# Performance work log

Hardware: AMD Instinct MI355X
Metric: run time of the kernel (lower is better)

The kernel has to match this reference:

```python
import jax, jax.numpy as jnp
import numpy as np

B, L, D, H, NL = 16, 256, 768, 12, 4
HD = D // H          # head size = 64; also edge-feature embedding dim
V, E, C, F = 30000, 50, 2, 3072
CLS_ID = 1


def _pos_emb(length, dim):
    # standard sinusoidal positional embedding [L, D]
    pos = jnp.arange(length, dtype=jnp.float32)[:, None]
    div = jnp.exp(-np.log(10000.0) * jnp.arange(0, dim, 2, dtype=jnp.float32) / dim)
    ang = pos * div[None, :]
    pe = jnp.zeros((length, dim), jnp.float32)
    return pe.at[:, 0::2].set(jnp.sin(ang)).at[:, 1::2].set(jnp.cos(ang))


def _ln(x, g, b, eps=1e-5):
    m = x.mean(-1, keepdims=True)
    v = x.var(-1, keepdims=True)
    return (x - m) * jax.lax.rsqrt(v + eps) * g + b


def setup_inputs() -> dict:
    key = jax.random.key(0)
    ks = jax.random.split(key, 16)
    s = 0.02
    word_ids = jax.random.randint(ks[0], (B, L), 0, V).at[:, 0].set(CLS_ID)
    batched_adj = jax.random.bernoulli(ks[1], 0.3, (B, L, L)) | jnp.eye(L, dtype=bool)[None]
    edge_types = jax.random.randint(ks[2], (B, L, L), 0, E)
    word_emb = (jax.random.normal(ks[3], (V, D)) * s).at[0].set(0.0)   # padding_idx=0
    edge_emb = (jax.random.normal(ks[4], (E, HD)) * s).at[0].set(0.0)  # padding_idx=0
    pw = lambda k, shp: jax.random.normal(k, shp) * s
    return {
        "word_ids": word_ids, "batched_adj": batched_adj, "edge_types": edge_types,
        "word_emb": word_emb, "edge_emb": edge_emb,
        "Wq": pw(ks[5], (NL, D, D)), "bq": jnp.zeros((NL, D)),
        "Wk": pw(ks[6], (NL, D, D)), "bk": jnp.zeros((NL, D)),
        "Wv": pw(ks[7], (NL, D, D)), "bv": jnp.zeros((NL, D)),
        "Wo": pw(ks[8], (NL, D, D)), "bo": jnp.zeros((NL, D)),
        "ln1_g": jnp.ones((NL, D)), "ln1_b": jnp.zeros((NL, D)),
        "W1": pw(ks[9], (NL, D, F)), "b1": jnp.zeros((NL, F)),
        "W2": pw(ks[10], (NL, F, D)), "b2": jnp.zeros((NL, D)),
        "ln2_g": jnp.ones((NL, D)), "ln2_b": jnp.zeros((NL, D)),
        "cls_W": pw(ks[11], (D, C)), "cls_b": jnp.zeros((C,)),
    }


def reference(word_ids, batched_adj, edge_types, word_emb, edge_emb,
              Wq, bq, Wk, bk, Wv, bv, Wo, bo, ln1_g, ln1_b,
              W1, b1, W2, b2, ln2_g, ln2_b, cls_W, cls_b):
    # node features: word embedding + positional embedding
    h = word_emb[word_ids] + _pos_emb(L, D)[None]          # [B,L,D]
    scale = 1.0 / np.sqrt(HD)
    eemb = edge_emb[edge_types]                             # [B,L,L,HD] edge key features
    neg = jnp.asarray(-1e9, h.dtype)
    mask = batched_adj[:, None]                             # [B,1,L,L]
    for l in range(NL):
        q = (h @ Wq[l] + bq[l]).reshape(B, L, H, HD)
        k = (h @ Wk[l] + bk[l]).reshape(B, L, H, HD)
        v = (h @ Wv[l] + bv[l]).reshape(B, L, H, HD)
        # scores: node-node + query . edge-key-feature, adjacency-masked
        scores = jnp.einsum('bihd,bjhd->bhij', q, k)
        scores = scores + jnp.einsum('bihd,bijd->bhij', q, eemb)
        scores = jnp.where(mask, scores * scale, neg)
        att = jax.nn.softmax(scores, axis=-1)               # [B,H,L,L]
        out = jnp.einsum('bhij,bjhd->bihd', att, v).reshape(B, L, D)
        h = _ln(h + (out @ Wo[l] + bo[l]), ln1_g[l], ln1_b[l])
        ff = jax.nn.relu(h @ W1[l] + b1[l]) @ W2[l] + b2[l]
        h = _ln(h + ff, ln2_g[l], ln2_b[l])
    cls_h = h[:, 0]                                         # CLS pooling
    logits = cls_h @ cls_W + cls_b                          # [B,C]
    return logits
```

## Files before the change

### kernel.cpp

```cpp
#include <hip/hip_runtime.h>
#include <hip/hip_bf16.h>

#define BB 16
#define LL 256
#define DD 768
#define HH 12
#define HDD 64
#define NLL 4
#define FF 3072
#define EE 50
#define QKVS 2304
#define TOKD ((size_t)BB * LL * DD)

typedef unsigned short ushort_t;
typedef __bf16 bf16x8 __attribute__((ext_vector_type(8)));
typedef float f32x4 __attribute__((ext_vector_type(4)));

__device__ __forceinline__ float b2f(ushort_t u) {
    union { unsigned int i; float f; } x; x.i = ((unsigned int)u) << 16; return x.f;
}
__device__ __forceinline__ ushort_t f2b(float f) {
    unsigned int u = __builtin_bit_cast(unsigned int, f);
    unsigned int r = u + 0x7fffu + ((u >> 16) & 1u);
    return (ushort_t)(r >> 16);
}

__device__ __forceinline__ void gl2lds16(const void* g, void* l) {
    __builtin_amdgcn_global_load_lds(
        (const __attribute__((address_space(1))) unsigned int*)g,
        (__attribute__((address_space(3))) unsigned int*)l,
        16, 0, 0);
}

__global__ __launch_bounds__(256) void transpose_f2b(
    const float* __restrict__ in, ushort_t* __restrict__ out, int R, int C,
    long inZ, long outZ)
{
    __shared__ ushort_t tile[32][33];
    in  += (long)blockIdx.z * inZ;
    out += (long)blockIdx.z * outZ;
    int c0 = blockIdx.x * 32, r0 = blockIdx.y * 32;
    int tx = threadIdx.x, ty = threadIdx.y;
#pragma unroll
    for (int i = 0; i < 32; i += 8)
        tile[ty + i][tx] = f2b(in[(long)(r0 + ty + i) * C + c0 + tx]);
    __syncthreads();
#pragma unroll
    for (int i = 0; i < 32; i += 8)
        out[(long)(c0 + ty + i) * R + r0 + tx] = tile[tx][ty + i];
}

__global__ __launch_bounds__(256) void fuse_bias_kernel(
    const float* __restrict__ bq, const float* __restrict__ bk,
    const float* __restrict__ bv, int l, float* __restrict__ out)
{
    int n = blockIdx.x * 256 + threadIdx.x;
    if (n >= QKVS) return;
    float v = (n < DD) ? bq[l * DD + n]
            : (n < 2 * DD) ? bk[l * DD + n - DD]
            : bv[l * DD + n - 2 * DD];
    out[n] = v;
}

__global__ __launch_bounds__(256) void embed_kernel(
    const int* __restrict__ wids, const float* __restrict__ wemb,
    float* __restrict__ hf, ushort_t* __restrict__ hb)
{
    long idx = (long)blockIdx.x * 256 + threadIdx.x;
    int d = (int)(idx % DD);
    int t = (int)(idx / DD);
    int lpos = t & (LL - 1);
    int wid = wids[t];
    float freq = expf(-9.210340371976184f * (float)(d & ~1) * (1.f / (float)DD));
    float ang = (float)lpos * freq;
    float pe = (d & 1) ? cosf(ang) : sinf(ang);
    float hv = wemb[(long)wid * DD + d] + pe;
    hf[idx] = hv;
    hb[idx] = f2b(hv);
}

__global__ __launch_bounds__(256) void gemm_bf16(
    const ushort_t* __restrict__ A, const ushort_t* __restrict__ Bt,
    const float* __restrict__ bias,
    ushort_t* __restrict__ outb, float* __restrict__ outf,
    int M, int N, int K, int Ksl, int relu)
{
    __shared__ __align__(16) ushort_t As[3][128 * 32];
    __shared__ __align__(16) ushort_t Bs[3][128 * 32];
    const int tid = threadIdx.x;
    const int wave = tid >> 6, lane = tid & 63;
    const int quad = lane >> 4, l16 = lane & 15;
    const int m0 = blockIdx.y * 128, n0 = blockIdx.x * 128;
    const int z = blockIdx.z;
    const int kbase = z * Ksl;
    const int wm = (wave >> 1) * 64, wn = (wave & 1) * 64;
    const ushort_t* Ab = A + (long)m0 * K;
    const ushort_t* Bb = Bt + (long)n0 * K;

    const int srow = tid >> 2, skc = (tid & 3) * 8;

    f32x4 acc[4][4];
#pragma unroll
    for (int mi = 0; mi < 4; ++mi)
#pragma unroll
        for (int ni = 0; ni < 4; ++ni) acc[mi][ni] = (f32x4){0.f, 0.f, 0.f, 0.f};

    const int nk = Ksl >> 5;

    auto stage = [&](int kt, ushort_t* Ad, ushort_t* Bd) {
        const int k0 = kbase + (kt << 5);
        const ushort_t* ga = &Ab[(long)srow * K + k0 + skc];
        const ushort_t* gb = &Bb[(long)srow * K + k0 + skc];
        char* la = (char*)Ad + wave * 1024;
        char* lb = (char*)Bd + wave * 1024;
        gl2lds16(ga, la);
        gl2lds16(gb, lb);
        gl2lds16(ga + (long)64 * K, la + 4096);
        gl2lds16(gb + (long)64 * K, lb + 4096);
    };

    ushort_t *A0 = As[0], *A1 = As[1], *A2 = As[2];
    ushort_t *B0 = Bs[0], *B1 = Bs[1], *B2 = Bs[2];

    stage(0, A0, B0);
    stage(1, A1, B1);

    for (int kt = 0; kt < nk; ++kt) {
        if (kt + 1 < nk) {
            asm volatile("s_waitcnt vmcnt(4)" ::: "memory");
        } else {
            asm volatile("s_waitcnt vmcnt(0)" ::: "memory");
        }
        __builtin_amdgcn_s_barrier();
        __builtin_amdgcn_sched_barrier(0);
        if (kt + 2 < nk) stage(kt + 2, A2, B2);
        bf16x8 af[4], bfr[4];
#pragma unroll
        for (int t = 0; t < 4; ++t)
            af[t] = *(const bf16x8*)&A0[(wm + t * 16 + l16) * 32 + quad * 8];
#pragma unroll
        for (int t = 0; t < 4; ++t)
            bfr[t] = *(const bf16x8*)&B0[(wn + t * 16 + l16) * 32 + quad * 8];
#pragma unroll
        for (int mi = 0; mi < 4; ++mi)
#pragma unroll
            for (int ni = 0; ni < 4; ++ni)
                acc[mi][ni] = __builtin_amdgcn_mfma_f32_16x16x32_bf16(
                    af[mi], bfr[ni], acc[mi][ni], 0, 0, 0);
        ushort_t* ta = A0; A0 = A1; A1 = A2; A2 = ta;
        ushort_t* tb = B0; B0 = B1; B1 = B2; B2 = tb;
    }

    float* outfz = outf ? outf + (size_t)z * M * N : nullptr;
#pragma unroll
    for (int ni = 0; ni < 4; ++ni) {
        int col = n0 + wn + ni * 16 + l16;
        float bv = (bias && z == 0) ? bias[col] : 0.f;
#pragma unroll
        for (int mi = 0; mi < 4; ++mi) {
#pragma unroll
            for (int r = 0; r < 4; ++r) {
                int row = m0 + wm + mi * 16 + quad * 4 + r;
                float vv = acc[mi][ni][r] + bv;
                if (relu) vv = fmaxf(vv, 0.f);
                if (outb) outb[(long)row * N + col] = f2b(vv);
                if (outfz) outfz[(long)row * N + col] = vv;
            }
        }
    }
}

#define QS_STR 72
#define VT_STR 264
#define P_STR  264
#define S_STR  257
#define PE_STR 53

__global__ __launch_bounds__(256) void attn_kernel(
    const ushort_t* __restrict__ qkv,
    const int* __restrict__ adjm, const int* __restrict__ etyp,
    const float* __restrict__ eemb, ushort_t* __restrict__ out)
{
    __shared__ __align__(16) char smem[64448];
    ushort_t* VT = (ushort_t*)smem;
    float*    S  = (float*)(smem + 33792);
    ushort_t* P  = (ushort_t*)(smem + 50240);
    float*    Pe = (float*)(smem + 58688);
    char*     U  = smem + 62080;
    float* invrow = (float*)(smem + 64384);
    ushort_t* Qs = (ushort_t*)U;
    float*    red = (float*)U;

    const int blk = blockIdx.x;
    const int qt = blk & 15;
    const int h  = (blk >> 4) % HH;
    const int b  = blk / (16 * HH);
    const int i0 = qt * 16;
    const int tid = threadIdx.x;
    const int wave = tid >> 6, lane = tid & 63;
    const int quad = lane >> 4, l16 = lane & 15;

    if (tid < 128) {
        int row = tid >> 3, d0 = (tid & 7) * 8;
        *(int4*)&Qs[row * QS_STR + d0] =
            *(const int4*)&qkv[((long)(b * LL + i0 + row)) * QKVS + h * HDD + d0];
    }
#pragma unroll
    for (int i = 0; i < 8; ++i) {
        int c = tid + i * 256;
        int j = c >> 3, d0 = (c & 7) * 8;
        int4 raw = *(const int4*)&qkv[((long)(b * LL + j)) * QKVS + 2 * DD + h * HDD + d0];
        const ushort_t* vals = (const ushort_t*)&raw;
#pragma unroll
        for (int u = 0; u < 8; ++u) VT[(d0 + u) * VT_STR + j] = vals[u];
    }
    __syncthreads();

    {
        int e = wave * 16 + l16;
        f32x4 acc = (f32x4){0.f, 0.f, 0.f, 0.f};
#pragma unroll
        for (int kk = 0; kk < 2; ++kk) {
            bf16x8 af = *(const bf16x8*)&Qs[l16 * QS_STR + kk * 32 + quad * 8];
            bf16x8 bf = (bf16x8){0, 0, 0, 0, 0, 0, 0, 0};
            if (e < EE) {
                const float* ep = &eemb[(long)e * HDD + kk * 32 + quad * 8];
#pragma unroll
                for (int u = 0; u < 8; ++u) bf[u] = (__bf16)ep[u];
            }
            acc = __builtin_amdgcn_mfma_f32_16x16x32_bf16(af, bf, acc, 0, 0, 0);
        }
        if (e < EE) {
#pragma unroll
            for (int r = 0; r < 4; ++r) Pe[(quad * 4 + r) * PE_STR + e] = acc[r];
        }
    }

#pragma unroll
    for (int jt = 0; jt < 4; ++jt) {
        int jtile = wave * 4 + jt;
        int j = jtile * 16 + l16;
        f32x4 acc = (f32x4){0.f, 0.f, 0.f, 0.f};
#pragma unroll
        for (int kk = 0; kk < 2; ++kk) {
            bf16x8 af = *(const bf16x8*)&Qs[l16 * QS_STR + kk * 32 + quad * 8];
            bf16x8 bf = *(const bf16x8*)&qkv[((long)(b * LL + j)) * QKVS + DD + h * HDD + kk * 32 + quad * 8];
            acc = __builtin_amdgcn_mfma_f32_16x16x32_bf16(af, bf, acc, 0, 0, 0);
        }
#pragma unroll
        for (int r = 0; r < 4; ++r)
            S[(quad * 4 + r) * S_STR + jtile * 16 + l16] = acc[r];
    }
    __syncthreads();

    {
        const int row = tid & 15, seg = tid >> 4;
        const int i = i0 + row;
        const int* etp = etyp + ((long)(b * LL + i)) * LL + seg * 16;
        const int* adp = adjm + ((long)(b * LL + i)) * LL + seg * 16;
        int etv[16], adv[16];
#pragma unroll
        for (int t = 0; t < 4; ++t) {
            *(int4*)&etv[t * 4] = *(const int4*)&etp[t * 4];
            *(int4*)&adv[t * 4] = *(const int4*)&adp[t * 4];
        }
        float vals[16];
        float pmax = -1e30f;
#pragma unroll
        for (int c = 0; c < 16; ++c) {
            float s = S[row * S_STR + seg * 16 + c];
            float pe = Pe[row * PE_STR + etv[c]];
            float vv = adv[c] ? (s + pe) * 0.125f : -1e30f;
            vals[c] = vv;
            pmax = fmaxf(pmax, vv);
        }
        red[row * 17 + seg] = pmax;
        __syncthreads();
        float m = -1e30f;
#pragma unroll
        for (int g = 0; g < 16; ++g) m = fmaxf(m, red[row * 17 + g]);
        float sum = 0.f;
#pragma unroll
        for (int c = 0; c < 16; ++c) {
            float p = __expf(vals[c] - m);
            ushort_t pb = f2b(p);
            sum += b2f(pb);
            P[row * P_STR + seg * 16 + c] = pb;
        }
        red[272 + row * 17 + seg] = sum;
        __syncthreads();
        if (tid < 16) {
            float tot = 0.f;
#pragma unroll
            for (int g = 0; g < 16; ++g) tot += red[272 + tid * 17 + g];
            invrow[tid] = 1.f / tot;
        }
        __syncthreads();
    }

    {
        f32x4 acc = (f32x4){0.f, 0.f, 0.f, 0.f};
#pragma unroll
        for (int kt = 0; kt < 8; ++kt) {
            bf16x8 af = *(const bf16x8*)&P[l16 * P_STR + kt * 32 + quad * 8];
            bf16x8 bf = *(const bf16x8*)&VT[(wave * 16 + l16) * VT_STR + kt * 32 + quad * 8];
            acc = __builtin_amdgcn_mfma_f32_16x16x32_bf16(af, bf, acc, 0, 0, 0);
        }
#pragma unroll
        for (int r = 0; r < 4; ++r) {
            int row = quad * 4 + r;
            float ov = acc[r] * invrow[row];
            out[((long)(b * LL + i0 + row)) * DD + h * HDD + wave * 16 + l16] = f2b(ov);
        }
    }
}

__global__ __launch_bounds__(256) void ln_kernel(
    float* __restrict__ hf, ushort_t* __restrict__ hb,
    const float* __restrict__ proj, int nparts,
    const float* __restrict__ g, const float* __restrict__ be)
{
    const int r = blockIdx.x, tid = threadIdx.x;
    const long rb = (long)r * DD;
    float x[3];
#pragma unroll
    for (int i = 0; i < 3; ++i) {
        int d = tid + i * 256;
        float t = hf[rb + d];
        for (int p = 0; p < nparts; ++p) t += proj[(size_t)p * TOKD + rb + d];
        x[i] = t;
    }
    float s = x[0] + x[1] + x[2];
    float s2 = x[0] * x[0] + x[1] * x[1] + x[2] * x[2];
#pragma unroll
    for (int o = 1; o < 64; o <<= 1) { s += __shfl_xor(s, o); s2 += __shfl_xor(s2, o); }
    __shared__ float rs[4], rq[4];
    int wave = tid >> 6;
    if ((tid & 63) == 0) { rs[wave] = s; rq[wave] = s2; }
    __syncthreads();
    float S  = rs[0] + rs[1] + rs[2] + rs[3];
    float S2 = rq[0] + rq[1] + rq[2] + rq[3];
    float mean = S * (1.f / (float)DD);
    float var  = S2 * (1.f / (float)DD) - mean * mean;
    float rstd = rsqrtf(var + 1e-5f);
#pragma unroll
    for (int i = 0; i < 3; ++i) {
        int d = tid + i * 256;
        float y = (x[i] - mean) * rstd * g[d] + be[d];
        hf[rb + d] = y;
        hb[rb + d] = f2b(y);
    }
}

__global__ __launch_bounds__(256) void cls_kernel(
    const float* __restrict__ hf, const float* __restrict__ W,
    const float* __restrict__ bias, float* __restrict__ out)
{
    int b = blockIdx.x, tid = threadIdx.x;
    const float* hr = hf + (long)b * LL * DD;
    float p0 = 0.f, p1 = 0.f;
    for (int d = tid; d < DD; d += 256) {
        float hv = hr[d];
        p0 = fmaf(hv, W[d * 2 + 0], p0);
        p1 = fmaf(hv, W[d * 2 + 1], p1);
    }
#pragma unroll
    for (int o = 1; o < 64; o <<= 1) { p0 += __shfl_xor(p0, o); p1 += __shfl_xor(p1, o); }
    __shared__ float r0[4], r1[4];
    int wave = tid >> 6;
    if ((tid & 63) == 0) { r0[wave] = p0; r1[wave] = p1; }
    __syncthreads();
    if (tid == 0) {
        out[b * 2 + 0] = r0[0] + r0[1] + r0[2] + r0[3] + bias[0];
        out[b * 2 + 1] = r1[0] + r1[1] + r1[2] + r1[3] + bias[1];
    }
}

extern "C" void kernel_launch(void* const* d_in, const int* in_sizes, int n_in,
                              void* d_out, int out_size, void* d_ws, size_t ws_size,
                              hipStream_t stream)
{
    const int* word_ids = (const int*)d_in[0];
    const int* adjm     = (const int*)d_in[1];
    const int* etyp     = (const int*)d_in[2];
    const float* wemb   = (const float*)d_in[3];
    const float* eemb   = (const float*)d_in[4];
    const float* Wq     = (const float*)d_in[5];
    const float* bq     = (const float*)d_in[6];
    const float* Wk     = (const float*)d_in[7];
    const float* bk     = (const float*)d_in[8];
    const float* Wv     = (const float*)d_in[9];
    const float* bv     = (const float*)d_in[10];
    const float* Wo     = (const float*)d_in[11];
    const float* bo     = (const float*)d_in[12];
    const float* ln1g   = (const float*)d_in[13];
    const float* ln1b   = (const float*)d_in[14];
    const float* W1     = (const float*)d_in[15];
    const float* b1     = (const float*)d_in[16];
    const float* W2     = (const float*)d_in[17];
    const float* b2     = (const float*)d_in[18];
    const float* ln2g   = (const float*)d_in[19];
    const float* ln2b   = (const float*)d_in[20];
    const float* clsW   = (const float*)d_in[21];
    const float* clsb   = (const float*)d_in[22];
    float* outp = (float*)d_out;

    char* ws = (char*)d_ws;
    size_t off = 0;
    auto alloc = [&](size_t bytes) -> char* {
        char* p = ws + off;
        off += (bytes + 255) & ~(size_t)255;
        return p;
    };
    const size_t DxD = (size_t)DD * DD;
    const size_t DxF = (size_t)DD * FF;
    const size_t TOK = (size_t)BB * LL;
    const size_t LSTR = (size_t)QKVS * DD + DxD + 2 * DxF;

    float*    hf  = (float*)alloc(TOK * DD * 4);
    ushort_t* hb  = (ushort_t*)alloc(TOK * DD * 2);
    ushort_t* qkv = (ushort_t*)alloc(TOK * QKVS * 2);
    ushort_t* ao  = (ushort_t*)alloc(TOK * DD * 2);
    float*    pjf = (float*)alloc(TOK * DD * 4);
    ushort_t* tw  = (ushort_t*)alloc(DxF * 2);
    ushort_t* ff1 = qkv;
    size_t tier1 = off + TOK * DD * 4;
    size_t tier2 = tier1 + 2 * TOK * DD * 4;
    size_t tier3 = tier2 + NLL * LSTR * 2;
    int S_o = 1, S_f = 1;
    ushort_t* cache = nullptr;
    if (ws_size >= tier1) { (void)alloc(TOK * DD * 4); S_o = 2; S_f = 2; }
    if (ws_size >= tier2) { (void)alloc(2 * TOK * DD * 4); S_f = 4; }
    if (ws_size >= tier3) { cache = (ushort_t*)alloc(NLL * LSTR * 2); }
    (void)in_sizes; (void)n_in; (void)out_size;

    dim3 tb(32, 8, 1);
    if (cache) {
        transpose_f2b<<<dim3(24, 24, NLL), tb, 0, stream>>>(Wq, cache,                 DD, DD, DxD, LSTR);
        transpose_f2b<<<dim3(24, 24, NLL), tb, 0, stream>>>(Wk, cache + DD * DD,       DD, DD, DxD, LSTR);
        transpose_f2b<<<dim3(24, 24, NLL), tb, 0, stream>>>(Wv, cache + 2 * DD * DD,   DD, DD, DxD, LSTR);
        transpose_f2b<<<dim3(24, 24, NLL), tb, 0, stream>>>(Wo, cache + 3 * DD * DD,   DD, DD, DxD, LSTR);
        transpose_f2b<<<dim3(96, 24, NLL), tb, 0, stream>>>(W1, cache + 4 * DD * DD,   DD, FF, DxF, LSTR);
        transpose_f2b<<<dim3(24, 96, NLL), tb, 0, stream>>>(W2, cache + 4 * DD * DD + DxF, FF, DD, DxF, LSTR);
    }

    embed_kernel<<<(int)(TOK * DD / 256), 256, 0, stream>>>(word_ids, wemb, hf, hb);

    const int M = (int)TOK;
    for (int l = 0; l < NLL; ++l) {
        const ushort_t *BtQKV, *BtO, *BtW1, *BtW2;
        if (cache) {
            const ushort_t* base = cache + (size_t)l * LSTR;
            BtQKV = base; BtO = base + 3 * DD * DD;
            BtW1 = base + 4 * DD * DD; BtW2 = base + 4 * DD * DD + DxF;
        } else {
            BtQKV = tw; BtO = tw; BtW1 = tw; BtW2 = tw;
        }
        fuse_bias_kernel<<<9, 256, 0, stream>>>(bq, bk, bv, l, pjf);
        if (!cache) {
            transpose_f2b<<<dim3(24, 24), tb, 0, stream>>>(Wq + (size_t)l * DxD, tw,               DD, DD, 0, 0);
            transpose_f2b<<<dim3(24, 24), tb, 0, stream>>>(Wk + (size_t)l * DxD, tw + DD * DD,     DD, DD, 0, 0);
            transpose_f2b<<<dim3(24, 24), tb, 0, stream>>>(Wv + (size_t)l * DxD, tw + 2 * DD * DD, DD, DD, 0, 0);
        }
        gemm_bf16<<<dim3(QKVS / 128, M / 128, 1), 256, 0, stream>>>(
            hb, BtQKV, pjf, qkv, nullptr, M, QKVS, DD, DD, 0);
        attn_kernel<<<BB * HH * 16, 256, 0, stream>>>(qkv, adjm, etyp, eemb, ao);
        if (!cache)
            transpose_f2b<<<dim3(24, 24), tb, 0, stream>>>(Wo + (size_t)l * DxD, tw, DD, DD, 0, 0);
        gemm_bf16<<<dim3(DD / 128, M / 128, S_o), 256, 0, stream>>>(
            ao, BtO, bo + l * DD, nullptr, pjf, M, DD, DD, DD / S_o, 0);
        ln_kernel<<<M, 256, 0, stream>>>(hf, hb, pjf, S_o, ln1g + l * DD, ln1b + l * DD);
        if (!cache)
            transpose_f2b<<<dim3(96, 24), tb, 0, stream>>>(W1 + (size_t)l * DxF, tw, DD, FF, 0, 0);
        gemm_bf16<<<dim3(FF / 128, M / 128, 1), 256, 0, stream>>>(
            hb, BtW1, b1 + l * FF, ff1, nullptr, M, FF, DD, DD, 1);
        if (!cache)
            transpose_f2b<<<dim3(24, 96), tb, 0, stream>>>(W2 + (size_t)l * DxF, tw, FF, DD, 0, 0);
        gemm_bf16<<<dim3(DD / 128, M / 128, S_f), 256, 0, stream>>>(
            ff1, BtW2, b2 + l * DD, nullptr, pjf, M, DD, FF, FF / S_f, 0);
        ln_kernel<<<M, 256, 0, stream>>>(hf, hb, pjf, S_f, ln2g + l * DD, ln2b + l * DD);
    }
    cls_kernel<<<BB, 256, 0, stream>>>(hf, clsW, clsb, outp);
}
```

Measured before the change: 1.213 ms.

## Prefetch V and mask loads into registers, alias LDS, swizzle V transpose, remap blocks

The attention kernel now issues its global loads for V, edge types and adjacency at kernel start, holding them in registers so their latency overlaps the score computation. The V transpose into shared memory is deferred until after the softmax, which lets VT alias the S/Pe region and shrinks LDS from about 64KB to about 44KB, allowing more resident workgroups. VT writes and reads use an XOR swizzle to reduce bank conflicts. Block IDs are remapped so neighbouring workgroups spread across batch/head, which may change cache locality. The cost is much higher register pressure from the 8 int4 V values plus 32 ints held across phases.

```diff
diff --git a/kernel.cpp b/kernel.cpp
--- a/kernel.cpp
+++ b/kernel.cpp
@@ -176,22 +176,31 @@
 #define S_STR  257
 #define PE_STR 53
 
+#define SM_S    0
+#define SM_PE   16448
+#define SM_VT   0
+#define SM_P    33792
+#define SM_U    42240
+#define SM_INV  44544
+#define SM_SZ   44608
+
 __global__ __launch_bounds__(256) void attn_kernel(
     const ushort_t* __restrict__ qkv,
     const int* __restrict__ adjm, const int* __restrict__ etyp,
     const float* __restrict__ eemb, ushort_t* __restrict__ out)
 {
-    __shared__ __align__(16) char smem[64448];
-    ushort_t* VT = (ushort_t*)smem;
-    float*    S  = (float*)(smem + 33792);
-    ushort_t* P  = (ushort_t*)(smem + 50240);
-    float*    Pe = (float*)(smem + 58688);
-    char*     U  = smem + 62080;
-    float* invrow = (float*)(smem + 64384);
+    __shared__ __align__(16) char smem[SM_SZ];
+    float*    S  = (float*)(smem + SM_S);
+    float*    Pe = (float*)(smem + SM_PE);
+    ushort_t* VT = (ushort_t*)(smem + SM_VT);
+    ushort_t* P  = (ushort_t*)(smem + SM_P);
+    char*     U  = smem + SM_U;
+    float* invrow = (float*)(smem + SM_INV);
     ushort_t* Qs = (ushort_t*)U;
     float*    red = (float*)U;
 
-    const int blk = blockIdx.x;
+    const int wgid = blockIdx.x;
+    const int blk = (wgid & 7) * ((BB * HH * 16) / 8) + (wgid >> 3);
     const int qt = blk & 15;
     const int h  = (blk >> 4) % HH;
     const int b  = blk / (16 * HH);
@@ -200,19 +209,29 @@
     const int wave = tid >> 6, lane = tid & 63;
     const int quad = lane >> 4, l16 = lane & 15;
 
+    const int vd0 = (tid & 7) * 8;
+    const int vj0 = tid >> 3;
+    int4 vreg[8];
+#pragma unroll
+    for (int i = 0; i < 8; ++i)
+        vreg[i] = *(const int4*)&qkv[((long)(b * LL + vj0 + 32 * i)) * QKVS + 2 * DD + h * HDD + vd0];
+
+    const int arow = tid & 15, aseg = tid >> 4;
+    int etv[16], adv[16];
+    {
+        const int* etp = etyp + ((long)(b * LL + i0 + arow)) * LL + aseg * 16;
+        const int* adp = adjm + ((long)(b * LL + i0 + arow)) * LL + aseg * 16;
+#pragma unroll
+        for (int t = 0; t < 4; ++t) {
+            *(int4*)&etv[t * 4] = *(const int4*)&etp[t * 4];
+            *(int4*)&adv[t * 4] = *(const int4*)&adp[t * 4];
+        }
+    }
+
     if (tid < 128) {
         int row = tid >> 3, d0 = (tid & 7) * 8;
         *(int4*)&Qs[row * QS_STR + d0] =
             *(const int4*)&qkv[((long)(b * LL + i0 + row)) * QKVS + h * HDD + d0];
-    }
-#pragma unroll
-    for (int i = 0; i < 8; ++i) {
-        int c = tid + i * 256;
-        int j = c >> 3, d0 = (c & 7) * 8;
-        int4 raw = *(const int4*)&qkv[((long)(b * LL + j)) * QKVS + 2 * DD + h * HDD + d0];
-        const ushort_t* vals = (const ushort_t*)&raw;
-#pragma unroll
-        for (int u = 0; u < 8; ++u) VT[(d0 + u) * VT_STR + j] = vals[u];
     }
     __syncthreads();
 
@@ -254,16 +273,7 @@
     __syncthreads();
 
     {
-        const int row = tid & 15, seg = tid >> 4;
-        const int i = i0 + row;
-        const int* etp = etyp + ((long)(b * LL + i)) * LL + seg * 16;
-        const int* adp = adjm + ((long)(b * LL + i)) * LL + seg * 16;
-        int etv[16], adv[16];
-#pragma unroll
-        for (int t = 0; t < 4; ++t) {
-            *(int4*)&etv[t * 4] = *(const int4*)&etp[t * 4];
-            *(int4*)&adv[t * 4] = *(const int4*)&adp[t * 4];
-        }
+        const int row = arow, seg = aseg;
         float vals[16];
         float pmax = -1e30f;
 #pragma unroll
@@ -289,6 +299,18 @@
         }
         red[272 + row * 17 + seg] = sum;
         __syncthreads();
+
+        {
+            const int vswz = (tid & 7) << 3;
+#pragma unroll
+            for (int i = 0; i < 8; ++i) {
+                const int jc = (vj0 + 32 * i) ^ vswz;
+                const ushort_t* vv = (const ushort_t*)&vreg[i];
+#pragma unroll
+                for (int u = 0; u < 8; ++u)
+                    VT[(vd0 + u) * VT_STR + jc] = vv[u];
+            }
+        }
         if (tid < 16) {
             float tot = 0.f;
 #pragma unroll
@@ -299,18 +321,20 @@
     }
 
     {
+        const int d = wave * 16 + l16;
+        const int rswz = ((d >> 3) & 7) << 3;
         f32x4 acc = (f32x4){0.f, 0.f, 0.f, 0.f};
 #pragma unroll
         for (int kt = 0; kt < 8; ++kt) {
             bf16x8 af = *(const bf16x8*)&P[l16 * P_STR + kt * 32 + quad * 8];
-            bf16x8 bf = *(const bf16x8*)&VT[(wave * 16 + l16) * VT_STR + kt * 32 + quad * 8];
+            bf16x8 bf = *(const bf16x8*)&VT[d * VT_STR + ((kt * 32 + quad * 8) ^ rswz)];
             acc = __builtin_amdgcn_mfma_f32_16x16x32_bf16(af, bf, acc, 0, 0, 0);
         }
 #pragma unroll
         for (int r = 0; r < 4; ++r) {
             int row = quad * 4 + r;
             float ov = acc[r] * invrow[row];
-            out[((long)(b * LL + i0 + row)) * DD + h * HDD + wave * 16 + l16] = f2b(ov);
+            out[((long)(b * LL + i0 + row)) * DD + h * HDD + d] = f2b(ov);
         }
     }
 }
```

Result: faster. 1.151 ms (-5.1%).
